# Kernel tuning notes

Hardware: AMD Instinct MI355X
Metric: run time of the kernel (lower is better)

## Reference

```python
import jax, jax.numpy as jnp
import numpy as np

B, Hh, Ww, D = 16, 74, 74, 768   # batch, patch-grid h, patch-grid w, feature dim
NH, NO = 8, 16                    # humans / objects per image
N_REL = 117                       # HOI relation classes


def _make_boxes(key, n):
    # valid boxes: x2 > x1, y2 > y1, all within [0, 74]
    k1, k2, k3, k4 = jax.random.split(key, 4)
    x1 = jax.random.randint(k1, (B, n), 0, Ww - 16)
    y1 = jax.random.randint(k2, (B, n), 0, Hh - 16)
    bw = jax.random.randint(k3, (B, n), 2, 16)
    bh = jax.random.randint(k4, (B, n), 2, 16)
    return jnp.stack([x1, y1, x1 + bw, y1 + bh], axis=-1).astype(jnp.int32)


def setup_inputs() -> dict:
    key = jax.random.key(0)
    ks = jax.random.split(key, 8)
    features = jax.random.normal(ks[0], (B, Hh, Ww, D), dtype=jnp.float32)
    human_boxes = _make_boxes(ks[1], NH)
    obj_boxes = _make_boxes(ks[2], NO)
    s = 0.02
    W1 = jax.random.normal(ks[3], (2 * D, 512), dtype=jnp.float32) * s
    b1 = jnp.zeros((512,), jnp.float32)
    W2 = jax.random.normal(ks[4], (512, 256), dtype=jnp.float32) * s
    b2 = jnp.zeros((256,), jnp.float32)
    W3 = jax.random.normal(ks[5], (256, N_REL), dtype=jnp.float32) * s
    b3 = jnp.zeros((N_REL,), jnp.float32)
    return {"features": features, "human_boxes": human_boxes, "obj_boxes": obj_boxes,
            "W1": W1, "b1": b1, "W2": W2, "b2": b2, "W3": W3, "b3": b3}


def _roi_mean(feats, boxes):
    # feats: [h, w, D]; boxes: [N, 4] int (x1, y1, x2, y2) in patch coords.
    # Mean of feats[y1:y2, x1:x2] via a summed-area table (vectorized, one pass).
    integ = jnp.cumsum(jnp.cumsum(feats, axis=0), axis=1)
    integ = jnp.pad(integ, ((1, 0), (1, 0), (0, 0)))  # [h+1, w+1, D]
    x1, y1, x2, y2 = boxes[:, 0], boxes[:, 1], boxes[:, 2], boxes[:, 3]
    s = integ[y2, x2] - integ[y1, x2] - integ[y2, x1] + integ[y1, x1]  # [N, D]
    area = ((y2 - y1) * (x2 - x1)).astype(feats.dtype)[:, None]
    return s / area


def reference(features, human_boxes, obj_boxes, W1, b1, W2, b2, W3, b3):
    hf = jax.vmap(_roi_mean)(features, human_boxes)  # [B, NH, D]
    of = jax.vmap(_roi_mean)(features, obj_boxes)    # [B, NO, D]
    # pairwise concat: for every (human, object) pair -> [B, NH, NO, 2D]
    pairs = jnp.concatenate([
        jnp.broadcast_to(hf[:, :, None, :], (B, NH, NO, D)),
        jnp.broadcast_to(of[:, None, :, :], (B, NH, NO, D)),
    ], axis=-1).reshape(B * NH * NO, 2 * D)
    h = jax.nn.relu(pairs @ W1 + b1)
    h = jax.nn.relu(h @ W2 + b2)
    return h @ W3 + b3  # [B*NH*NO, 117] relation scores
```

## Files before the change

kernel.cpp:

```cpp
#include <hip/hip_runtime.h>

#define BB   16
#define HH   74
#define WW   74
#define DD   768
#define NHh  8
#define NOo  16
#define NREL 117
#define NKQ  8
#define KCH  96
#define ABSTRIDE (384 * 512)

#define FMA4(A, s, W) \
    A.x = fmaf((s), (W).x, A.x); A.y = fmaf((s), (W).y, A.y); \
    A.z = fmaf((s), (W).z, A.z); A.w = fmaf((s), (W).w, A.w);


__global__ __launch_bounds__(512) void roi_gemm1_kernel(const float* __restrict__ feats,
                                                        const int* __restrict__ hboxes,
                                                        const int* __restrict__ oboxes,
                                                        const float* __restrict__ W1,
                                                        float* __restrict__ AB)
{
    __shared__ __align__(16) float part[15][4][KCH];
    __shared__ __align__(16) float xs[4][KCH];
    __shared__ __align__(16) float red[4][4][512];
    int r0 = blockIdx.x * 4;
    int kq = blockIdx.y;
    int t = threadIdx.x;

    if (t < 360) {
        int c4 = t % 24;
        int s  = t / 24;
        for (int r = 0; r < 4; ++r) {
            int row = r0 + r;
            const int* box = (row < 128) ? (hboxes + row * 4) : (oboxes + (row - 128) * 4);
            int x1 = box[0], y1 = box[1], x2 = box[2], y2 = box[3];
            if (s < y2 - y1) {
                int b = (row < 128) ? (row >> 3) : ((row - 128) >> 4);
                int y = y1 + s;
                const float4* rp = (const float4*)(feats + (size_t)((b * HH + y) * WW) * DD + kq * KCH) + c4;
                float4 a0 = make_float4(0.f, 0.f, 0.f, 0.f);
                float4 a1 = make_float4(0.f, 0.f, 0.f, 0.f);
                float4 a2 = make_float4(0.f, 0.f, 0.f, 0.f);
                float4 a3 = make_float4(0.f, 0.f, 0.f, 0.f);
                int x = x1;
                for (; x + 3 < x2; x += 4) {
                    float4 v0 = rp[(size_t)(x + 0) * 192];
                    float4 v1 = rp[(size_t)(x + 1) * 192];
                    float4 v2 = rp[(size_t)(x + 2) * 192];
                    float4 v3 = rp[(size_t)(x + 3) * 192];
                    a0.x += v0.x; a0.y += v0.y; a0.z += v0.z; a0.w += v0.w;
                    a1.x += v1.x; a1.y += v1.y; a1.z += v1.z; a1.w += v1.w;
                    a2.x += v2.x; a2.y += v2.y; a2.z += v2.z; a2.w += v2.w;
                    a3.x += v3.x; a3.y += v3.y; a3.z += v3.z; a3.w += v3.w;
                }
                for (; x < x2; ++x) {
                    float4 v0 = rp[(size_t)x * 192];
                    a0.x += v0.x; a0.y += v0.y; a0.z += v0.z; a0.w += v0.w;
                }
                a0.x += a1.x + a2.x + a3.x;
                a0.y += a1.y + a2.y + a3.y;
                a0.z += a1.z + a2.z + a3.z;
                a0.w += a1.w + a2.w + a3.w;
                *(float4*)&part[s][r][c4 * 4] = a0;
            }
        }
    }
    __syncthreads();

    for (int idx = t; idx < 4 * KCH; idx += 512) {
        int r = idx / KCH;
        int k = idx - r * KCH;
        int row = r0 + r;
        const int* box = (row < 128) ? (hboxes + row * 4) : (oboxes + (row - 128) * 4);
        int bh = box[3] - box[1];
        float inv_area = 1.0f / (float)(bh * (box[2] - box[0]));
        float ssum = 0.f;
        for (int s = 0; s < bh; ++s) ssum += part[s][r][k];
        xs[r][k] = ssum * inv_area;
    }
    __syncthreads();

    int c  = t & 127;
    int kh = t >> 7;
    int kb = kh * 24;
    const float* W1p = W1 + ((size_t)(((r0 < 128) ? 0 : DD) + kq * KCH + kb)) * 512 + 4 * c;

    float4 a[4];
#pragma unroll
    for (int r = 0; r < 4; ++r) a[r] = make_float4(0.f, 0.f, 0.f, 0.f);

    for (int kk = 0; kk < 24; kk += 8) {
        float4 w[8];
#pragma unroll
        for (int u = 0; u < 8; ++u) w[u] = *(const float4*)(W1p + (size_t)(kk + u) * 512);
#pragma unroll
        for (int r = 0; r < 4; ++r) {
            float4 x0 = *(const float4*)&xs[r][kb + kk];
            float4 x1 = *(const float4*)&xs[r][kb + kk + 4];
            float xv[8] = {x0.x, x0.y, x0.z, x0.w, x1.x, x1.y, x1.z, x1.w};
#pragma unroll
            for (int u = 0; u < 8; ++u) { FMA4(a[r], xv[u], w[u]); }
        }
    }
#pragma unroll
    for (int r = 0; r < 4; ++r) *(float4*)&red[kh][r][4 * c] = a[r];
    __syncthreads();

    float* ABq = AB + (size_t)kq * ABSTRIDE;
    for (int idx = t; idx < 4 * 512; idx += 512) {
        int r = idx >> 9;
        int cc = idx & 511;
        ABq[(size_t)(r0 + r) * 512 + cc] = red[0][r][cc] + red[1][r][cc]
                                         + red[2][r][cc] + red[3][r][cc];
    }
}

__global__ __launch_bounds__(1024) void mlp_kernel(const float* __restrict__ AB,
                                                   const float* __restrict__ b1,
                                                   const float* __restrict__ W2,
                                                   const float* __restrict__ b2,
                                                   const float* __restrict__ W3,
                                                   const float* __restrict__ b3,
                                                   float* __restrict__ out)
{
    __shared__ __align__(16) float h1[8][512];
    __shared__ __align__(16) float red[8][8][256];
    __shared__ __align__(16) float h2[8][256];
    int p0 = blockIdx.x * 8;
    int t = threadIdx.x;

    for (int idx = t; idx < 8 * 512; idx += 1024) {
        int r = idx >> 9;
        int k = idx & 511;
        int p = p0 + r;
        int rowA = p >> 4;
        int rowB = 128 + (p >> 7) * 16 + (p & 15);
        float v = b1[k];
#pragma unroll
        for (int q = 0; q < NKQ; ++q)
            v += AB[(size_t)q * ABSTRIDE + (size_t)rowA * 512 + k]
               + AB[(size_t)q * ABSTRIDE + (size_t)rowB * 512 + k];
        h1[r][k] = v > 0.f ? v : 0.f;
    }
    __syncthreads();

    {
        int c   = t & 63;
        int kq2 = (t >> 6) & 7;
        int rh  = t >> 9;
        int kbase = kq2 * 64;
        const float* W2p = W2 + (size_t)kbase * 256 + 4 * c;
        float4 a[4];
#pragma unroll
        for (int r = 0; r < 4; ++r) a[r] = make_float4(0.f, 0.f, 0.f, 0.f);

        for (int kk = 0; kk < 64; kk += 4) {
            float4 w[4];
#pragma unroll
            for (int u = 0; u < 4; ++u) w[u] = *(const float4*)(W2p + (size_t)(kk + u) * 256);
#pragma unroll
            for (int r = 0; r < 4; ++r) {
                float4 x0 = *(const float4*)&h1[rh * 4 + r][kbase + kk];
                float xv[4] = {x0.x, x0.y, x0.z, x0.w};
#pragma unroll
                for (int u = 0; u < 4; ++u) { FMA4(a[r], xv[u], w[u]); }
            }
        }
#pragma unroll
        for (int r = 0; r < 4; ++r) *(float4*)&red[kq2][rh * 4 + r][4 * c] = a[r];
    }
    __syncthreads();

    for (int idx = t; idx < 8 * 256; idx += 1024) {
        int r = idx >> 8;
        int cc = idx & 255;
        float s = b2[cc];
#pragma unroll
        for (int q = 0; q < 8; ++q) s += red[q][r][cc];
        h2[r][cc] = s > 0.f ? s : 0.f;
    }
    __syncthreads();

    float* pr = &red[0][0][0];
    if (t < 8 * NREL) {
        int o = t % NREL;
        int jq = t / NREL;
        float acc[8] = {};
        const float* W3p = W3 + o;
        for (int j = jq * 32; j < jq * 32 + 32; j += 4) {
            float w[4];
#pragma unroll
            for (int u = 0; u < 4; ++u) w[u] = W3p[(size_t)(j + u) * NREL];
#pragma unroll
            for (int r = 0; r < 8; ++r) {
                float4 x0 = *(const float4*)&h2[r][j];
                acc[r] = fmaf(x0.x, w[0], acc[r]); acc[r] = fmaf(x0.y, w[1], acc[r]);
                acc[r] = fmaf(x0.z, w[2], acc[r]); acc[r] = fmaf(x0.w, w[3], acc[r]);
            }
        }
#pragma unroll
        for (int r = 0; r < 8; ++r) pr[(jq * 8 + r) * NREL + o] = acc[r];
    }
    __syncthreads();

    if (t < 8 * NREL) {
        int r = t / NREL;
        int o = t - r * NREL;
        float s = b3[o];
#pragma unroll
        for (int q = 0; q < 8; ++q) s += pr[(q * 8 + r) * NREL + o];
        out[(size_t)(p0 + r) * NREL + o] = s;
    }
}

extern "C" void kernel_launch(void* const* d_in, const int* in_sizes, int n_in,
                              void* d_out, int out_size, void* d_ws, size_t ws_size,
                              hipStream_t stream) {
    const float* feats  = (const float*)d_in[0];
    const int*   hboxes = (const int*)d_in[1];
    const int*   oboxes = (const int*)d_in[2];
    const float* W1     = (const float*)d_in[3];
    const float* b1     = (const float*)d_in[4];
    const float* W2     = (const float*)d_in[5];
    const float* b2     = (const float*)d_in[6];
    const float* W3     = (const float*)d_in[7];
    const float* b3     = (const float*)d_in[8];
    float* out = (float*)d_out;

    float* AB = (float*)d_ws;

    roi_gemm1_kernel<<<dim3(96, NKQ), dim3(512), 0, stream>>>(feats, hboxes, oboxes, W1, AB);
    mlp_kernel<<<dim3(256), dim3(1024), 0, stream>>>(AB, b1, W2, b2, W3, b3, out);
}
```

Baseline: 48.76 us.

## Halve GEMM1 K-split, vectorize h1 build, widen unrolls, add occupancy hints

In the ROI/GEMM1 kernel, only 256 threads now do the W1 product, each over 48 K rows instead of 24, which halves the shared reduction buffer and the final sum. Both kernels gain minimum-blocks hints in their launch bounds. The mlp kernel builds h1 with float4 loads instead of scalar ones, and its W2 and W3 loops are unrolled by 8. The aim is less shared memory, less reduction work and more memory-level parallelism, at the cost of half the threads sitting idle during GEMM1 and possible register pressure or spills from the occupancy hints.

```diff
diff --git a/kernel.cpp b/kernel.cpp
--- a/kernel.cpp
+++ b/kernel.cpp
@@ -16,15 +16,15 @@
     A.z = fmaf((s), (W).z, A.z); A.w = fmaf((s), (W).w, A.w);
 
 
-__global__ __launch_bounds__(512) void roi_gemm1_kernel(const float* __restrict__ feats,
-                                                        const int* __restrict__ hboxes,
-                                                        const int* __restrict__ oboxes,
-                                                        const float* __restrict__ W1,
-                                                        float* __restrict__ AB)
+__global__ __launch_bounds__(512, 6) void roi_gemm1_kernel(const float* __restrict__ feats,
+                                                           const int* __restrict__ hboxes,
+                                                           const int* __restrict__ oboxes,
+                                                           const float* __restrict__ W1,
+                                                           float* __restrict__ AB)
 {
     __shared__ __align__(16) float part[15][4][KCH];
     __shared__ __align__(16) float xs[4][KCH];
-    __shared__ __align__(16) float red[4][4][512];
+    __shared__ __align__(16) float red[2][4][512];
     int r0 = blockIdx.x * 4;
     int kq = blockIdx.y;
     int t = threadIdx.x;
@@ -82,48 +82,49 @@
     }
     __syncthreads();
 
-    int c  = t & 127;
-    int kh = t >> 7;
-    int kb = kh * 24;
-    const float* W1p = W1 + ((size_t)(((r0 < 128) ? 0 : DD) + kq * KCH + kb)) * 512 + 4 * c;
-
-    float4 a[4];
-#pragma unroll
-    for (int r = 0; r < 4; ++r) a[r] = make_float4(0.f, 0.f, 0.f, 0.f);
-
-    for (int kk = 0; kk < 24; kk += 8) {
-        float4 w[8];
-#pragma unroll
-        for (int u = 0; u < 8; ++u) w[u] = *(const float4*)(W1p + (size_t)(kk + u) * 512);
-#pragma unroll
-        for (int r = 0; r < 4; ++r) {
-            float4 x0 = *(const float4*)&xs[r][kb + kk];
-            float4 x1 = *(const float4*)&xs[r][kb + kk + 4];
-            float xv[8] = {x0.x, x0.y, x0.z, x0.w, x1.x, x1.y, x1.z, x1.w};
-#pragma unroll
-            for (int u = 0; u < 8; ++u) { FMA4(a[r], xv[u], w[u]); }
-        }
-    }
-#pragma unroll
-    for (int r = 0; r < 4; ++r) *(float4*)&red[kh][r][4 * c] = a[r];
+    if (t < 256) {
+        int c  = t & 127;
+        int kh = t >> 7;
+        int kb = kh * 48;
+        const float* W1p = W1 + ((size_t)(((r0 < 128) ? 0 : DD) + kq * KCH + kb)) * 512 + 4 * c;
+
+        float4 a[4];
+#pragma unroll
+        for (int r = 0; r < 4; ++r) a[r] = make_float4(0.f, 0.f, 0.f, 0.f);
+
+        for (int kk = 0; kk < 48; kk += 8) {
+            float4 w[8];
+#pragma unroll
+            for (int u = 0; u < 8; ++u) w[u] = *(const float4*)(W1p + (size_t)(kk + u) * 512);
+#pragma unroll
+            for (int r = 0; r < 4; ++r) {
+                float4 x0 = *(const float4*)&xs[r][kb + kk];
+                float4 x1 = *(const float4*)&xs[r][kb + kk + 4];
+                float xv[8] = {x0.x, x0.y, x0.z, x0.w, x1.x, x1.y, x1.z, x1.w};
+#pragma unroll
+                for (int u = 0; u < 8; ++u) { FMA4(a[r], xv[u], w[u]); }
+            }
+        }
+#pragma unroll
+        for (int r = 0; r < 4; ++r) *(float4*)&red[kh][r][4 * c] = a[r];
+    }
     __syncthreads();
 
     float* ABq = AB + (size_t)kq * ABSTRIDE;
     for (int idx = t; idx < 4 * 512; idx += 512) {
         int r = idx >> 9;
         int cc = idx & 511;
-        ABq[(size_t)(r0 + r) * 512 + cc] = red[0][r][cc] + red[1][r][cc]
-                                         + red[2][r][cc] + red[3][r][cc];
+        ABq[(size_t)(r0 + r) * 512 + cc] = red[0][r][cc] + red[1][r][cc];
     }
 }
 
-__global__ __launch_bounds__(1024) void mlp_kernel(const float* __restrict__ AB,
-                                                   const float* __restrict__ b1,
-                                                   const float* __restrict__ W2,
-                                                   const float* __restrict__ b2,
-                                                   const float* __restrict__ W3,
-                                                   const float* __restrict__ b3,
-                                                   float* __restrict__ out)
+__global__ __launch_bounds__(1024, 4) void mlp_kernel(const float* __restrict__ AB,
+                                                      const float* __restrict__ b1,
+                                                      const float* __restrict__ W2,
+                                                      const float* __restrict__ b2,
+                                                      const float* __restrict__ W3,
+                                                      const float* __restrict__ b3,
+                                                      float* __restrict__ out)
 {
     __shared__ __align__(16) float h1[8][512];
     __shared__ __align__(16) float red[8][8][256];
@@ -131,18 +132,23 @@
     int p0 = blockIdx.x * 8;
     int t = threadIdx.x;
 
-    for (int idx = t; idx < 8 * 512; idx += 1024) {
-        int r = idx >> 9;
-        int k = idx & 511;
+    {
+        int r  = t >> 7;
+        int k4 = t & 127;
         int p = p0 + r;
         int rowA = p >> 4;
         int rowB = 128 + (p >> 7) * 16 + (p & 15);
-        float v = b1[k];
-#pragma unroll
-        for (int q = 0; q < NKQ; ++q)
-            v += AB[(size_t)q * ABSTRIDE + (size_t)rowA * 512 + k]
-               + AB[(size_t)q * ABSTRIDE + (size_t)rowB * 512 + k];
-        h1[r][k] = v > 0.f ? v : 0.f;
+        float4 v = ((const float4*)b1)[k4];
+#pragma unroll
+        for (int q = 0; q < NKQ; ++q) {
+            float4 av = ((const float4*)(AB + (size_t)q * ABSTRIDE + (size_t)rowA * 512))[k4];
+            float4 bv = ((const float4*)(AB + (size_t)q * ABSTRIDE + (size_t)rowB * 512))[k4];
+            v.x += av.x + bv.x; v.y += av.y + bv.y;
+            v.z += av.z + bv.z; v.w += av.w + bv.w;
+        }
+        v.x = v.x > 0.f ? v.x : 0.f; v.y = v.y > 0.f ? v.y : 0.f;
+        v.z = v.z > 0.f ? v.z : 0.f; v.w = v.w > 0.f ? v.w : 0.f;
+        *(float4*)&h1[r][k4 * 4] = v;
     }
     __syncthreads();
 
@@ -156,16 +162,17 @@
 #pragma unroll
         for (int r = 0; r < 4; ++r) a[r] = make_float4(0.f, 0.f, 0.f, 0.f);
 
-        for (int kk = 0; kk < 64; kk += 4) {
-            float4 w[4];
-#pragma unroll
-            for (int u = 0; u < 4; ++u) w[u] = *(const float4*)(W2p + (size_t)(kk + u) * 256);
+        for (int kk = 0; kk < 64; kk += 8) {
+            float4 w[8];
+#pragma unroll
+            for (int u = 0; u < 8; ++u) w[u] = *(const float4*)(W2p + (size_t)(kk + u) * 256);
 #pragma unroll
             for (int r = 0; r < 4; ++r) {
                 float4 x0 = *(const float4*)&h1[rh * 4 + r][kbase + kk];
-                float xv[4] = {x0.x, x0.y, x0.z, x0.w};
-#pragma unroll
-                for (int u = 0; u < 4; ++u) { FMA4(a[r], xv[u], w[u]); }
+                float4 x1 = *(const float4*)&h1[rh * 4 + r][kbase + kk + 4];
+                float xv[8] = {x0.x, x0.y, x0.z, x0.w, x1.x, x1.y, x1.z, x1.w};
+#pragma unroll
+                for (int u = 0; u < 8; ++u) { FMA4(a[r], xv[u], w[u]); }
             }
         }
 #pragma unroll
@@ -189,15 +196,18 @@
         int jq = t / NREL;
         float acc[8] = {};
         const float* W3p = W3 + o;
-        for (int j = jq * 32; j < jq * 32 + 32; j += 4) {
-            float w[4];
-#pragma unroll
-            for (int u = 0; u < 4; ++u) w[u] = W3p[(size_t)(j + u) * NREL];
+        for (int j = jq * 32; j < jq * 32 + 32; j += 8) {
+            float w[8];
+#pragma unroll
+            for (int u = 0; u < 8; ++u) w[u] = W3p[(size_t)(j + u) * NREL];
 #pragma unroll
             for (int r = 0; r < 8; ++r) {
                 float4 x0 = *(const float4*)&h2[r][j];
+                float4 x1 = *(const float4*)&h2[r][j + 4];
                 acc[r] = fmaf(x0.x, w[0], acc[r]); acc[r] = fmaf(x0.y, w[1], acc[r]);
                 acc[r] = fmaf(x0.z, w[2], acc[r]); acc[r] = fmaf(x0.w, w[3], acc[r]);
+                acc[r] = fmaf(x1.x, w[4], acc[r]); acc[r] = fmaf(x1.y, w[5], acc[r]);
+                acc[r] = fmaf(x1.z, w[6], acc[r]); acc[r] = fmaf(x1.w, w[7], acc[r]);
             }
         }
 #pragma unroll
```

After: 43.84 us, median of 2. -10.1%, faster.
